# Kernel optimization log

Measured on AMD Instinct MI355X. Metric: run time of the kernel, lower is better.

Reference implementation:

```python
import jax, jax.numpy as jnp
import numpy as np

INPUT_SIZE = 512
HIDDEN_SIZE = 1024
SEQ_LEN = 512
BATCH = 64


def _xavier(key, shape):
    fan_out, fan_in = shape
    limit = float(np.sqrt(6.0 / (fan_in + fan_out)))
    return jax.random.uniform(key, shape, jnp.float32, -limit, limit)


def setup_inputs() -> dict:
    key = jax.random.key(0)
    ks = jax.random.split(key, 10)
    return {
        "x_seq": jax.random.normal(ks[0], (SEQ_LEN, BATCH, INPUT_SIZE), jnp.float32),
        "h": jax.random.normal(ks[1], (BATCH, HIDDEN_SIZE), jnp.float32),
        "U_c": _xavier(ks[2], (HIDDEN_SIZE, INPUT_SIZE)),
        "w_c": jax.random.normal(ks[3], (HIDDEN_SIZE,), jnp.float32),
        "b_c": jax.random.normal(ks[4], (HIDDEN_SIZE,), jnp.float32),
        "U_a": _xavier(ks[5], (HIDDEN_SIZE, INPUT_SIZE)),
        "w_a": jax.random.normal(ks[6], (HIDDEN_SIZE,), jnp.float32),
        "b_a": jax.random.normal(ks[7], (HIDDEN_SIZE,), jnp.float32),
        "U_h": _xavier(ks[8], (HIDDEN_SIZE, INPUT_SIZE)),
        "b_h": jax.random.normal(ks[9], (HIDDEN_SIZE,), jnp.float32),
    }


def reference(x_seq, h, U_c, w_c, b_c, U_a, w_a, b_a, U_h, b_h):
    # Precompute all input projections in one big batched GEMM each:
    # (S, B, I) @ (I, H) -> (S, B, H)
    xc = jnp.einsum("sbi,hi->sbh", x_seq, U_c) + b_c
    xa = jnp.einsum("sbi,hi->sbh", x_seq, U_a) + b_a
    xh = jnp.einsum("sbi,hi->sbh", x_seq, U_h) + b_h

    def step(h, proj):
        pc, pa, ph = proj
        c = jax.nn.sigmoid(pc + w_c * h)
        a = 1.0 + jnp.tanh(pa + w_a * h)
        h_new = c * h + (1.0 - c) * jnp.tanh(ph + a * h)
        return h_new, h_new

    hn, y_seq = jax.lax.scan(step, h, (xc, xa, xh))
    return y_seq, hn
```

## Files before the change

### kernel.cpp

```cpp
#include <hip/hip_runtime.h>
#include <hip/hip_bf16.h>
#include <stdint.h>

#define SEQLEN 512
#define NBATCH 64
#define KDIM   512
#define HDIM   1024
#define MTOT   (SEQLEN * NBATCH)
#define NTOT   (3 * HDIM)
#define STRIDE (NBATCH * HDIM)

typedef __attribute__((ext_vector_type(4))) float f32x4;
typedef _Float16 f16x8 __attribute__((ext_vector_type(8)));

__global__ __launch_bounds__(256) void cvt_x(const float* __restrict__ x,
                                             _Float16* __restrict__ xh,
                                             _Float16* __restrict__ xl) {
    int i = blockIdx.x * 256 + threadIdx.x;
    const float4* s = (const float4*)(x + (size_t)i * 8);
    float4 a = s[0], b = s[1];
    float v[8] = {a.x, a.y, a.z, a.w, b.x, b.y, b.z, b.w};
    f16x8 hi, lo;
#pragma unroll
    for (int j = 0; j < 8; ++j) {
        _Float16 h = (_Float16)v[j];
        hi[j] = h;
        lo[j] = (_Float16)(v[j] - (float)h);
    }
    *(f16x8*)(xh + (size_t)i * 8) = hi;
    *(f16x8*)(xl + (size_t)i * 8) = lo;
}

__global__ __launch_bounds__(256) void cvt_u(const float* __restrict__ Uc,
                                             const float* __restrict__ Ua,
                                             const float* __restrict__ Uh,
                                             _Float16* __restrict__ uh,
                                             _Float16* __restrict__ ul) {
    int i = blockIdx.x * 256 + threadIdx.x;
    int n = i >> 6;
    int kb = (i & 63) * 8;
    const float* src = (n < HDIM) ? (Uc + (size_t)n * KDIM)
                     : (n < 2 * HDIM) ? (Ua + (size_t)(n - HDIM) * KDIM)
                     : (Uh + (size_t)(n - 2 * HDIM) * KDIM);
    const float4* s = (const float4*)(src + kb);
    float4 a = s[0], b = s[1];
    float v[8] = {a.x, a.y, a.z, a.w, b.x, b.y, b.z, b.w};
    f16x8 hi, lo;
#pragma unroll
    for (int j = 0; j < 8; ++j) {
        _Float16 h = (_Float16)v[j];
        hi[j] = h;
        lo[j] = (_Float16)(v[j] - (float)h);
    }
    *(f16x8*)(uh + (size_t)n * KDIM + kb) = hi;
    *(f16x8*)(ul + (size_t)n * KDIM + kb) = lo;
}

#define BM 256
#define BN 256
#define BK 32
#define NT_N (NTOT / BN)
#define GRID ((MTOT / BM) * NT_N)
#define KT_N (KDIM / BK)

__device__ __forceinline__ void gload16(const _Float16* g, _Float16* l) {
    __builtin_amdgcn_global_load_lds((const __attribute__((address_space(1))) void*)g,
                                     (__attribute__((address_space(3))) void*)l,
                                     16, 0, 0);
}

__device__ __forceinline__ f32x4 mfma16(f16x8 a, f16x8 b, f32x4 c) {
    return __builtin_amdgcn_mfma_f32_16x16x32_f16(a, b, c, 0, 0, 0);
}

__global__ __launch_bounds__(512, 2) void gemm_f16x2(const _Float16* __restrict__ Ah,
                                                     const _Float16* __restrict__ Al,
                                                     const _Float16* __restrict__ Bh,
                                                     const _Float16* __restrict__ Bl,
                                                     float* __restrict__ pc,
                                                     float* __restrict__ pa,
                                                     float* __restrict__ ph) {
    __shared__ _Float16 lds[2][4][BM * BK];

    int bid  = blockIdx.x;
    int bm   = bid / NT_N;
    int bn   = bid % NT_N;
    int tid  = threadIdx.x;
    int lane = tid & 63;
    int wave = tid >> 6;
    int wr   = wave >> 2;
    int wc   = wave & 3;

    size_t row_off = (size_t)(tid >> 2) * KDIM
                   + (size_t)(((tid & 3) ^ ((tid >> 3) & 3)) * 8);
    const _Float16* gAh = Ah + (size_t)bm * BM * KDIM + row_off;
    const _Float16* gAl = Al + (size_t)bm * BM * KDIM + row_off;
    const _Float16* gBh = Bh + (size_t)bn * BN * KDIM + row_off;
    const _Float16* gBl = Bl + (size_t)bn * BN * KDIM + row_off;
    const size_t HPAN = (size_t)128 * KDIM;
    int t8 = tid * 8;

#define STAGE(b, kt) do { int _g = (kt) * BK;                                  \
    gload16(gAh + _g,        &lds[b][0][t8]);                                  \
    gload16(gAh + HPAN + _g, &lds[b][0][t8 + 4096]);                           \
    gload16(gAl + _g,        &lds[b][1][t8]);                                  \
    gload16(gAl + HPAN + _g, &lds[b][1][t8 + 4096]);                           \
    gload16(gBh + _g,        &lds[b][2][t8]);                                  \
    gload16(gBh + HPAN + _g, &lds[b][2][t8 + 4096]);                           \
    gload16(gBl + _g,        &lds[b][3][t8]);                                  \
    gload16(gBl + HPAN + _g, &lds[b][3][t8 + 4096]); } while (0)

    f32x4 acc[8][4];
#pragma unroll
    for (int i = 0; i < 8; ++i)
#pragma unroll
        for (int j = 0; j < 4; ++j)
            acc[i][j] = (f32x4){0.f, 0.f, 0.f, 0.f};

    int ro = lane & 15;
    int ko = ((lane >> 4) ^ ((lane >> 1) & 3)) * 8;

    f16x8 a_[4][2], b_[2][2];

#define READ_A(mh) _Pragma("unroll")                                           \
    for (int i = 0; i < 4; ++i) {                                              \
        int row = wr * 128 + ((mh) * 4 + i) * 16 + ro;                         \
        a_[i][0] = *(const f16x8*)(&lds[cur][0][row * BK + ko]);               \
        a_[i][1] = *(const f16x8*)(&lds[cur][1][row * BK + ko]);               \
    }
#define READ_B(nh) _Pragma("unroll")                                           \
    for (int j = 0; j < 2; ++j) {                                              \
        int row = wc * 64 + ((nh) * 2 + j) * 16 + ro;                          \
        b_[j][0] = *(const f16x8*)(&lds[cur][2][row * BK + ko]);               \
        b_[j][1] = *(const f16x8*)(&lds[cur][3][row * BK + ko]);               \
    }
#define MFMA_Q(mh, nh) _Pragma("unroll")                                       \
    for (int i = 0; i < 4; ++i) _Pragma("unroll")                              \
        for (int j = 0; j < 2; ++j) {                                          \
            f32x4 c = acc[(mh) * 4 + i][(nh) * 2 + j];                         \
            c = mfma16(a_[i][0], b_[j][1], c);                                 \
            c = mfma16(a_[i][1], b_[j][0], c);                                 \
            c = mfma16(a_[i][0], b_[j][0], c);                                 \
            acc[(mh) * 4 + i][(nh) * 2 + j] = c;                               \
        }
#define LGKM0 do { asm volatile("s_waitcnt lgkmcnt(0)" ::: "memory");          \
                   __builtin_amdgcn_sched_barrier(0); } while (0)

    STAGE(0, 0);

    for (int kt = 0; kt < KT_N; ++kt) {
        int cur = kt & 1;
        if (kt < KT_N - 1) {
            STAGE(1 - cur, kt + 1);
            asm volatile("s_waitcnt vmcnt(8)" ::: "memory");
        } else {
            asm volatile("s_waitcnt vmcnt(0)" ::: "memory");
        }
        __builtin_amdgcn_s_barrier();
        asm volatile("" ::: "memory");

        READ_A(0); READ_B(0);
        LGKM0;
        __builtin_amdgcn_s_setprio(1); MFMA_Q(0, 0); __builtin_amdgcn_s_setprio(0);
        READ_B(1);
        __builtin_amdgcn_s_barrier();
        LGKM0;
        __builtin_amdgcn_s_setprio(1); MFMA_Q(0, 1); __builtin_amdgcn_s_setprio(0);
        READ_A(1);
        __builtin_amdgcn_s_barrier();
        LGKM0;
        __builtin_amdgcn_s_setprio(1); MFMA_Q(1, 1); __builtin_amdgcn_s_setprio(0);
        READ_B(0);
        __builtin_amdgcn_s_barrier();
        LGKM0;
        __builtin_amdgcn_s_setprio(1); MFMA_Q(1, 0); __builtin_amdgcn_s_setprio(0);
        __builtin_amdgcn_s_barrier();
    }

    int n0 = bn * BN;
    float* outp; int nb;
    if (n0 < HDIM)            { outp = pc; nb = n0; }
    else if (n0 < 2 * HDIM)   { outp = pa; nb = n0 - HDIM; }
    else                      { outp = ph; nb = n0 - 2 * HDIM; }

#pragma unroll
    for (int ai = 0; ai < 8; ++ai)
#pragma unroll
        for (int bj = 0; bj < 4; ++bj) {
            int m = bm * BM + wr * 128 + ai * 16 + (lane >> 4) * 4;
            int n = nb + wc * 64 + bj * 16 + (lane & 15);
#pragma unroll
            for (int r = 0; r < 4; ++r)
                outp[(size_t)(m + r) * HDIM + n] = acc[ai][bj][r];
        }
#undef STAGE
#undef READ_A
#undef READ_B
#undef MFMA_Q
#undef LGKM0
}

__global__ __launch_bounds__(256) void recur(const float* __restrict__ pc_a,
                                             const float* __restrict__ pa_a,
                                             float* out,
                                             const float* __restrict__ h0,
                                             const float* __restrict__ wc_,
                                             const float* __restrict__ bc_,
                                             const float* __restrict__ wa_,
                                             const float* __restrict__ ba_,
                                             const float* __restrict__ bh_) {
    int idx = blockIdx.x * 256 + threadIdx.x;
    int j = idx & (HDIM - 1);
    float h  = h0[idx];
    float wc = wc_[j], bc = bc_[j];
    float wa = wa_[j], ba = ba_[j];
    float bh = bh_[j];

#define PF 16
    float pc[PF], pa[PF], ph[PF];
#pragma unroll
    for (int u = 0; u < PF; ++u) {
        pc[u] = pc_a[(size_t)u * STRIDE + idx];
        pa[u] = pa_a[(size_t)u * STRIDE + idx];
        ph[u] = out [(size_t)u * STRIDE + idx];
    }

    for (int sb = 0; sb < SEQLEN; sb += PF) {
#pragma unroll
        for (int u = 0; u < PF; ++u) {
            int s = sb + u;
            float vc = pc[u], va = pa[u], vh = ph[u];
            int sp = s + PF; sp = (sp < SEQLEN) ? sp : (SEQLEN - 1);
            pc[u] = pc_a[(size_t)sp * STRIDE + idx];
            pa[u] = pa_a[(size_t)sp * STRIDE + idx];
            ph[u] = out [(size_t)sp * STRIDE + idx];

            float zc = (vc + bc) + wc * h;
            float za = (va + ba) + wa * h;
            float c  = 1.0f / (1.0f + expf(-zc));
            float a  = 1.0f + tanhf(za);
            float ht = tanhf((vh + bh) + a * h);
            h = c * h + (1.0f - c) * ht;
            out[(size_t)s * STRIDE + idx] = h;
        }
    }
    out[(size_t)SEQLEN * STRIDE + idx] = h;
}

extern "C" void kernel_launch(void* const* d_in, const int* in_sizes, int n_in,
                              void* d_out, int out_size, void* d_ws, size_t ws_size,
                              hipStream_t stream) {
    const float* x_seq = (const float*)d_in[0];
    const float* h0    = (const float*)d_in[1];
    const float* U_c   = (const float*)d_in[2];
    const float* w_c   = (const float*)d_in[3];
    const float* b_c   = (const float*)d_in[4];
    const float* U_a   = (const float*)d_in[5];
    const float* w_a   = (const float*)d_in[6];
    const float* b_a   = (const float*)d_in[7];
    const float* U_h   = (const float*)d_in[8];
    const float* b_h   = (const float*)d_in[9];
    float* out = (float*)d_out;

    char* ws = (char*)d_ws;
    const size_t MB = 1024 * 1024;
    float*    ws_pc = (float*)ws;
    float*    ws_pa = (float*)(ws + 128 * MB);
    _Float16* x_hi  = (_Float16*)(ws + 256 * MB);
    _Float16* x_lo  = (_Float16*)(ws + 288 * MB);
    _Float16* u_hi  = (_Float16*)(ws + 320 * MB);
    _Float16* u_lo  = (_Float16*)(ws + 323 * MB);

    cvt_x<<<dim3(MTOT * KDIM / 8 / 256), dim3(256), 0, stream>>>(x_seq, x_hi, x_lo);
    cvt_u<<<dim3(NTOT * KDIM / 8 / 256), dim3(256), 0, stream>>>(U_c, U_a, U_h, u_hi, u_lo);
    gemm_f16x2<<<dim3(GRID), dim3(512), 0, stream>>>(
        x_hi, x_lo, u_hi, u_lo, ws_pc, ws_pa, out);
    recur<<<dim3(STRIDE / 256), dim3(256), 0, stream>>>(ws_pc, ws_pa, out, h0,
                                                        w_c, b_c, w_a, b_a, b_h);
}
```

Before: 482.8 us.

## Restructure GEMM main loop to interleave next-tile loads with MFMA halves

The split-fp16 GEMM main loop changes from four quarter-steps, each separated by a barrier, to two MFMA halves. All B fragments are read up front, and the A-plane and B-plane global-to-LDS prefetches for the next k-tile are issued between the halves. It now waits for all outstanding loads with a single barrier per iteration, trading the earlier vmcnt(8) overlap for fewer barriers and more B registers held. The recurrence kernel's register prefetch depth also doubles from 16 to 32 steps, putting more loads in flight at the cost of more VGPRs.

```diff
diff --git a/kernel.cpp b/kernel.cpp
--- a/kernel.cpp
+++ b/kernel.cpp
@@ -100,15 +100,9 @@
     const size_t HPAN = (size_t)128 * KDIM;
     int t8 = tid * 8;
 
-#define STAGE(b, kt) do { int _g = (kt) * BK;                                  \
-    gload16(gAh + _g,        &lds[b][0][t8]);                                  \
-    gload16(gAh + HPAN + _g, &lds[b][0][t8 + 4096]);                           \
-    gload16(gAl + _g,        &lds[b][1][t8]);                                  \
-    gload16(gAl + HPAN + _g, &lds[b][1][t8 + 4096]);                           \
-    gload16(gBh + _g,        &lds[b][2][t8]);                                  \
-    gload16(gBh + HPAN + _g, &lds[b][2][t8 + 4096]);                           \
-    gload16(gBl + _g,        &lds[b][3][t8]);                                  \
-    gload16(gBl + HPAN + _g, &lds[b][3][t8 + 4096]); } while (0)
+#define SPAIR(buf, plane, gp, kt) do { int _g = (kt) * BK;                     \
+    gload16((gp) + _g,        &lds[buf][plane][t8]);                           \
+    gload16((gp) + HPAN + _g, &lds[buf][plane][t8 + 4096]); } while (0)
 
     f32x4 acc[8][4];
 #pragma unroll
@@ -120,7 +114,7 @@
     int ro = lane & 15;
     int ko = ((lane >> 4) ^ ((lane >> 1) & 3)) * 8;
 
-    f16x8 a_[4][2], b_[2][2];
+    f16x8 a_[4][2], b_[4][2];
 
 #define READ_A(mh) _Pragma("unroll")                                           \
     for (int i = 0; i < 4; ++i) {                                              \
@@ -128,53 +122,46 @@
         a_[i][0] = *(const f16x8*)(&lds[cur][0][row * BK + ko]);               \
         a_[i][1] = *(const f16x8*)(&lds[cur][1][row * BK + ko]);               \
     }
-#define READ_B(nh) _Pragma("unroll")                                           \
-    for (int j = 0; j < 2; ++j) {                                              \
-        int row = wc * 64 + ((nh) * 2 + j) * 16 + ro;                          \
+#define READ_B() _Pragma("unroll")                                             \
+    for (int j = 0; j < 4; ++j) {                                              \
+        int row = wc * 64 + j * 16 + ro;                                       \
         b_[j][0] = *(const f16x8*)(&lds[cur][2][row * BK + ko]);               \
         b_[j][1] = *(const f16x8*)(&lds[cur][3][row * BK + ko]);               \
     }
-#define MFMA_Q(mh, nh) _Pragma("unroll")                                       \
+#define MFMA_HALF(mh) _Pragma("unroll")                                        \
     for (int i = 0; i < 4; ++i) _Pragma("unroll")                              \
-        for (int j = 0; j < 2; ++j) {                                          \
-            f32x4 c = acc[(mh) * 4 + i][(nh) * 2 + j];                         \
-            c = mfma16(a_[i][0], b_[j][1], c);                                 \
-            c = mfma16(a_[i][1], b_[j][0], c);                                 \
-            c = mfma16(a_[i][0], b_[j][0], c);                                 \
-            acc[(mh) * 4 + i][(nh) * 2 + j] = c;                               \
+        for (int j = 0; j < 4; ++j) {                                          \
+            f32x4 c = acc[(mh) * 4 + i][j];                                    \
+            c = mfma16(a_[i][0], b_[j][1], c);                      \
+            c = mfma16(a_[i][1], b_[j][0], c);                      \
+            c = mfma16(a_[i][0], b_[j][0], c);                      \
+            acc[(mh) * 4 + i][j] = c;                                          \
         }
-#define LGKM0 do { asm volatile("s_waitcnt lgkmcnt(0)" ::: "memory");          \
-                   __builtin_amdgcn_sched_barrier(0); } while (0)
-
-    STAGE(0, 0);
+
+    SPAIR(0, 0, gAh, 0);
+    SPAIR(0, 1, gAl, 0);
+    SPAIR(0, 2, gBh, 0);
+    SPAIR(0, 3, gBl, 0);
 
     for (int kt = 0; kt < KT_N; ++kt) {
-        int cur = kt & 1;
-        if (kt < KT_N - 1) {
-            STAGE(1 - cur, kt + 1);
-            asm volatile("s_waitcnt vmcnt(8)" ::: "memory");
-        } else {
-            asm volatile("s_waitcnt vmcnt(0)" ::: "memory");
-        }
+        int cur = kt & 1, nxt = 1 - cur;
+        bool pre = (kt < KT_N - 1);
+        __builtin_amdgcn_sched_barrier(0);
+        asm volatile("s_waitcnt vmcnt(0)" ::: "memory");
         __builtin_amdgcn_s_barrier();
-        asm volatile("" ::: "memory");
-
-        READ_A(0); READ_B(0);
-        LGKM0;
-        __builtin_amdgcn_s_setprio(1); MFMA_Q(0, 0); __builtin_amdgcn_s_setprio(0);
-        READ_B(1);
-        __builtin_amdgcn_s_barrier();
-        LGKM0;
-        __builtin_amdgcn_s_setprio(1); MFMA_Q(0, 1); __builtin_amdgcn_s_setprio(0);
+        __builtin_amdgcn_sched_barrier(0);
+
+        READ_B();
+        READ_A(0);
+        if (pre) { SPAIR(nxt, 0, gAh, kt + 1); SPAIR(nxt, 1, gAl, kt + 1); }
+        __builtin_amdgcn_s_setprio(1);
+        MFMA_HALF(0);
+        __builtin_amdgcn_s_setprio(0);
         READ_A(1);
-        __builtin_amdgcn_s_barrier();
-        LGKM0;
-        __builtin_amdgcn_s_setprio(1); MFMA_Q(1, 1); __builtin_amdgcn_s_setprio(0);
-        READ_B(0);
-        __builtin_amdgcn_s_barrier();
-        LGKM0;
-        __builtin_amdgcn_s_setprio(1); MFMA_Q(1, 0); __builtin_amdgcn_s_setprio(0);
-        __builtin_amdgcn_s_barrier();
+        if (pre) { SPAIR(nxt, 2, gBh, kt + 1); SPAIR(nxt, 3, gBl, kt + 1); }
+        __builtin_amdgcn_s_setprio(1);
+        MFMA_HALF(1);
+        __builtin_amdgcn_s_setprio(0);
     }
 
     int n0 = bn * BN;
@@ -193,11 +180,10 @@
             for (int r = 0; r < 4; ++r)
                 outp[(size_t)(m + r) * HDIM + n] = acc[ai][bj][r];
         }
-#undef STAGE
+#undef SPAIR
 #undef READ_A
 #undef READ_B
-#undef MFMA_Q
-#undef LGKM0
+#undef MFMA_HALF
 }
 
 __global__ __launch_bounds__(256) void recur(const float* __restrict__ pc_a,
@@ -216,7 +202,7 @@
     float wa = wa_[j], ba = ba_[j];
     float bh = bh_[j];
 
-#define PF 16
+#define PF 32
     float pc[PF], pa[PF], ph[PF];
 #pragma unroll
     for (int u = 0; u < PF; ++u) {
```

After: 462.7 us. 4.2% less time.
